# Kernel optimization log

Hardware: AMD Instinct MI355X
Metric: run time of the kernel (lower is better)

The kernel has to match this reference:

```python
import math
import jax, jax.numpy as jnp
import numpy as np

D_MODEL = 1024
D_FF = 4096
NUM_EXPERTS = 8
TOP_K = 2
CAP_FACTOR = 1.0
AUX_COEF = 0.01
Z_COEF = 0.0


def setup_inputs() -> dict:
    key = jax.random.key(0)
    ks = jax.random.split(key, 6)
    x = jax.random.normal(ks[0], (4, 2048, D_MODEL), dtype=jnp.float32)
    router_w = jax.random.normal(ks[1], (D_MODEL, NUM_EXPERTS), dtype=jnp.float32) / math.sqrt(D_MODEL)
    router_b = jnp.zeros((NUM_EXPERTS,), dtype=jnp.float32)
    w1 = jax.random.normal(ks[2], (NUM_EXPERTS, D_MODEL, D_FF), dtype=jnp.float32) / math.sqrt(D_MODEL)
    w3 = jax.random.normal(ks[3], (NUM_EXPERTS, D_MODEL, D_FF), dtype=jnp.float32) / math.sqrt(D_MODEL)
    w2 = jax.random.normal(ks[4], (NUM_EXPERTS, D_FF, D_MODEL), dtype=jnp.float32) / math.sqrt(D_FF)
    return {"x": x, "router_w": router_w, "router_b": router_b, "w1": w1, "w3": w3, "w2": w2}


def reference(x, router_w, router_b, w1, w3, w2):
    b, s, d = x.shape
    E, k = NUM_EXPERTS, TOP_K
    T = b * s
    x_flat = x.reshape(T, d)

    # ---- router ----
    logits = x_flat @ router_w + router_b                      # [T, E]
    logits_f32 = logits.astype(jnp.float32)
    probs = jax.nn.softmax(logits_f32, axis=-1)                # [T, E]
    topk_p, topk_i = jax.lax.top_k(probs, k)                   # [T, k]
    topk_p = topk_p / jnp.clip(topk_p.sum(-1, keepdims=True), 1e-9)  # normalize_gates
    gate = topk_p.reshape(-1)                                  # [T*k]
    expert_idx = topk_i.reshape(-1)                            # [T*k]

    # ---- aux loss (load balance + z-loss) ----
    importance = probs.mean(axis=0)                            # [E]
    load = jnp.bincount(topk_i[:, 0], length=E).astype(jnp.float32) / T
    lb_loss = (importance * load).sum() * float(E)
    z_loss = jnp.mean(jnp.square(jax.nn.logsumexp(logits_f32, axis=-1)))
    aux_loss = (AUX_COEF * lb_loss + Z_COEF * z_loss).astype(x.dtype)

    # ---- capacity-based dispatch ----
    N = T * k
    cap = max(1, int(math.ceil(CAP_FACTOR * N / E)))
    x_rep = jnp.repeat(x_flat, k, axis=0)                      # [N, d]
    order = jnp.argsort(expert_idx)                            # stable sort by expert
    e_sorted = expert_idx[order]
    x_sorted = x_rep[order]
    g_sorted = gate[order].astype(x.dtype)
    counts = jnp.bincount(e_sorted, length=E)
    starts = jnp.concatenate([jnp.zeros((1,), counts.dtype), jnp.cumsum(counts)[:-1]])
    pos = jnp.arange(N, dtype=counts.dtype) - starts[e_sorted]   # rank within expert group
    keep = pos < cap
    slot = jnp.where(keep, e_sorted * cap + pos, E * cap)      # dropped tokens -> dump row

    buf = jnp.zeros((E * cap + 1, d), dtype=x.dtype).at[slot].set(x_sorted)
    buf = buf[: E * cap].reshape(E, cap, d)                    # [E, C, d]

    # ---- grouped SwiGLU experts ----
    h = jax.nn.silu(jnp.einsum('ecd,edf->ecf', buf, w1)) * jnp.einsum('ecd,edf->ecf', buf, w3)
    y = jnp.einsum('ecf,efd->ecd', h, w2).reshape(E * cap, d)

    # ---- combine ----
    gathered = y[jnp.minimum(slot, E * cap - 1)]
    out_sorted = jnp.where(keep[:, None], gathered, 0.0) * g_sorted[:, None]
    inv = jnp.argsort(order)
    out = out_sorted[inv].reshape(T, k, d).sum(axis=1)
    return out.reshape(b, s, d), aux_loss
```

## Files before the change

### kernel.cpp

```cpp
#include <hip/hip_runtime.h>
#include <hip/hip_bf16.h>
#include <math.h>

constexpr int kT    = 8192;
constexpr int kD    = 1024;
constexpr int kF    = 4096;
constexpr int kE    = 8;
constexpr int kN    = kT * 2;
constexpr int kCap  = 2048;
constexpr int kECap = kE * kCap;

constexpr int kRouterBlocks = kT / 4;
constexpr int kT13Blocks    = (kF / 64) * (kD / 64) * 16;
constexpr int kT2Blocks     = (kD / 64) * (kF / 64) * 8;

typedef __attribute__((ext_vector_type(8))) short bf16x8;
typedef __attribute__((ext_vector_type(4))) float f32x4;

__device__ __forceinline__ void gload16(const __hip_bfloat16* g, __hip_bfloat16* l) {
  auto gp = (const __attribute__((address_space(1))) __hip_bfloat16*)g;
  auto lp = (__attribute__((address_space(3))) __hip_bfloat16*)l;
  __builtin_amdgcn_global_load_lds((const __attribute__((address_space(1))) void*)gp,
                                   (__attribute__((address_space(3))) void*)lp,
                                   16, 0, 0);
}

#define SYNC_VM(N) do { __builtin_amdgcn_sched_barrier(0); \
  asm volatile("s_waitcnt vmcnt(" #N ")" ::: "memory"); \
  __builtin_amdgcn_s_barrier(); \
  asm volatile("" ::: "memory"); } while (0)

__device__ __forceinline__ void transpose_body(const float* __restrict__ s,
                                               __hip_bfloat16* __restrict__ d,
                                               int R, int C, int bx, int by) {
  __shared__ float tile[64][65];
  const int c0 = bx * 64, r0 = by * 64;
  const int tid = threadIdx.x;
  const int lr = tid >> 4, lc4 = (tid & 15) * 4;
#pragma unroll
  for (int p = 0; p < 4; ++p) {
    int r = p * 16 + lr;
    float4 v = *(const float4*)(s + (size_t)(r0 + r) * C + c0 + lc4);
    tile[r][lc4] = v.x; tile[r][lc4 + 1] = v.y; tile[r][lc4 + 2] = v.z; tile[r][lc4 + 3] = v.w;
  }
  __syncthreads();
  const int c = tid >> 2, rc = (tid & 3) * 16;
  union { __hip_bfloat16 h[16]; bf16x8 v[2]; } o;
#pragma unroll
  for (int i = 0; i < 16; ++i) o.h[i] = __float2bfloat16(tile[rc + i][c]);
  __hip_bfloat16* drow = d + (size_t)(c0 + c) * R + r0 + rc;
  *(bf16x8*)drow = o.v[0];
  *(bf16x8*)(drow + 8) = o.v[1];
}

__global__ __launch_bounds__(256)
void prep_kernel(const float* __restrict__ x, const float* __restrict__ rw,
                 const float* __restrict__ rb, int* __restrict__ e_idx,
                 float* __restrict__ gates, float* __restrict__ probs_out,
                 const float* __restrict__ w1, const float* __restrict__ w3,
                 const float* __restrict__ w2, __hip_bfloat16* __restrict__ w1t,
                 __hip_bfloat16* __restrict__ w3t, __hip_bfloat16* __restrict__ w2t) {
  int bid = blockIdx.x;
  if (bid < kRouterBlocks) {
    int t = bid * 4 + (threadIdx.x >> 6);
    int lane = threadIdx.x & 63;
    const float* xr = x + (size_t)t * kD;
    float acc[8];
#pragma unroll
    for (int e = 0; e < 8; ++e) acc[e] = 0.f;
    for (int i = 0; i < kD / 256; ++i) {
      int d = i * 256 + lane * 4;
      float4 xv = *(const float4*)(xr + d);
#pragma unroll
      for (int j = 0; j < 4; ++j) {
        float xs = (j == 0) ? xv.x : (j == 1) ? xv.y : (j == 2) ? xv.z : xv.w;
        const float4* w4 = (const float4*)(rw + (size_t)(d + j) * 8);
        float4 wa = w4[0], wb = w4[1];
        acc[0] += xs * wa.x; acc[1] += xs * wa.y; acc[2] += xs * wa.z; acc[3] += xs * wa.w;
        acc[4] += xs * wb.x; acc[5] += xs * wb.y; acc[6] += xs * wb.z; acc[7] += xs * wb.w;
      }
    }
#pragma unroll
    for (int off = 32; off >= 1; off >>= 1) {
#pragma unroll
      for (int e = 0; e < 8; ++e) acc[e] += __shfl_xor(acc[e], off);
    }
    if (lane == 0) {
      float l[8], m = -1e30f;
#pragma unroll
      for (int e = 0; e < 8; ++e) { l[e] = acc[e] + rb[e]; m = fmaxf(m, l[e]); }
      float p[8], s = 0.f;
#pragma unroll
      for (int e = 0; e < 8; ++e) { p[e] = __expf(l[e] - m); s += p[e]; }
      float inv = 1.f / s;
#pragma unroll
      for (int e = 0; e < 8; ++e) p[e] *= inv;
      int i1 = 0;
#pragma unroll
      for (int e = 1; e < 8; ++e) if (p[e] > p[i1]) i1 = e;
      int i2 = (i1 == 0) ? 1 : 0;
#pragma unroll
      for (int e = 0; e < 8; ++e) if (e != i1 && e != i2 && p[e] > p[i2]) i2 = e;
      float den = fmaxf(p[i1] + p[i2], 1e-9f);
      e_idx[2 * t] = i1; e_idx[2 * t + 1] = i2;
      gates[2 * t] = p[i1] / den; gates[2 * t + 1] = p[i2] / den;
      float4* po = (float4*)(probs_out + (size_t)t * 8);
      po[0] = make_float4(p[0], p[1], p[2], p[3]);
      po[1] = make_float4(p[4], p[5], p[6], p[7]);
    }
    return;
  }
  const float* src; __hip_bfloat16* dst; int R, C, bx, by;
  bid -= kRouterBlocks;
  if (bid < kT13Blocks) {
    bx = bid & 63; by = (bid >> 6) & 15;
    int z = bid >> 10;
    R = kD; C = kF;
    size_t mat = (size_t)kD * kF;
    src = ((z < 8) ? w1 : w3) + (size_t)(z & 7) * mat;
    dst = ((z < 8) ? w1t : w3t) + (size_t)(z & 7) * mat;
  } else {
    bid -= kT13Blocks;
    bx = bid & 15; by = (bid >> 4) & 63;
    int e2 = bid >> 10;
    R = kF; C = kD;
    size_t mat = (size_t)kF * kD;
    src = w2 + (size_t)e2 * mat;
    dst = w2t + (size_t)e2 * mat;
  }
  transpose_body(src, dst, R, C, bx, by);
}

__global__ __launch_bounds__(1024)
void aux_kernel(const float* __restrict__ probs, const int* __restrict__ e_idx,
                float* __restrict__ aux_out) {
  int tid = threadIdx.x, lane = tid & 63, wave = tid >> 6;
  float imp[8];
  int cnt[8];
#pragma unroll
  for (int e = 0; e < 8; ++e) { imp[e] = 0.f; cnt[e] = 0; }
  for (int t = tid; t < kT; t += 1024) {
    const float4* p4 = (const float4*)(probs + (size_t)t * 8);
    float4 a = p4[0], b = p4[1];
    imp[0] += a.x; imp[1] += a.y; imp[2] += a.z; imp[3] += a.w;
    imp[4] += b.x; imp[5] += b.y; imp[6] += b.z; imp[7] += b.w;
    ++cnt[e_idx[2 * t] & 7];
  }
#pragma unroll
  for (int off = 32; off >= 1; off >>= 1) {
#pragma unroll
    for (int e = 0; e < 8; ++e) {
      imp[e] += __shfl_xor(imp[e], off);
      cnt[e] += __shfl_xor(cnt[e], off);
    }
  }
  __shared__ float simp[16][8];
  __shared__ int scnt[16][8];
  if (lane == 0) {
#pragma unroll
    for (int e = 0; e < 8; ++e) { simp[wave][e] = imp[e]; scnt[wave][e] = cnt[e]; }
  }
  __syncthreads();
  if (tid == 0) {
    float lb = 0.f;
    for (int e = 0; e < 8; ++e) {
      float I = 0.f; int C = 0;
      for (int w = 0; w < 16; ++w) { I += simp[w][e]; C += scnt[w][e]; }
      lb += (I / (float)kT) * ((float)C / (float)kT);
    }
    aux_out[0] = 0.01f * lb * (float)kE;
  }
}

__global__ __launch_bounds__(256)
void rank_kernel(const int* __restrict__ e_idx, int* __restrict__ slot_of,
                 int* __restrict__ token_of) {
  int e = blockIdx.x;
  __shared__ int wave_sum[4];
  __shared__ int running;
  int tid = threadIdx.x, lane = tid & 63, wave = tid >> 6;
  if (tid == 0) running = 0;
  __syncthreads();
  for (int base = 0; base < kN; base += 256) {
    int i = base + tid;
    bool f = (e_idx[i] == e);
    unsigned long long m = __ballot(f);
    int wpre = __popcll(m & ((1ull << lane) - 1ull));
    if (lane == 0) wave_sum[wave] = __popcll(m);
    __syncthreads();
    int woff = 0;
    for (int w = 0; w < wave; ++w) woff += wave_sum[w];
    int r = running;
    if (f) {
      int p = r + woff + wpre;
      if (p < kCap) {
        slot_of[i] = e * kCap + p;
        token_of[e * kCap + p] = i >> 1;
      } else {
        slot_of[i] = -1;
      }
    }
    __syncthreads();
    if (tid == 0) running = r + wave_sum[0] + wave_sum[1] + wave_sum[2] + wave_sum[3];
    __syncthreads();
  }
  for (int p = running + tid; p < kCap; p += 256)
    token_of[e * kCap + p] = -1;
}

struct __attribute__((aligned(8))) bf16x4s { __hip_bfloat16 v[4]; };

__global__ __launch_bounds__(64)
void gather_kernel(const float* __restrict__ x, const int* __restrict__ token_of,
                   __hip_bfloat16* __restrict__ buf) {
  int slot = blockIdx.x, lane = threadIdx.x;
  int t = token_of[slot];
  __hip_bfloat16* br = buf + (size_t)slot * kD;
  if (t >= 0) {
    const float* xr = x + (size_t)t * kD;
#pragma unroll
    for (int j = 0; j < 4; ++j) {
      int dd = (j * 64 + lane) * 4;
      float4 v = *(const float4*)(xr + dd);
      bf16x4s o;
      o.v[0] = __float2bfloat16(v.x); o.v[1] = __float2bfloat16(v.y);
      o.v[2] = __float2bfloat16(v.z); o.v[3] = __float2bfloat16(v.w);
      *(bf16x4s*)(br + dd) = o;
    }
  } else {
    bf16x4s z;
    z.v[0] = z.v[1] = z.v[2] = z.v[3] = __float2bfloat16(0.f);
#pragma unroll
    for (int j = 0; j < 4; ++j) *(bf16x4s*)(br + (j * 64 + lane) * 4) = z;
  }
}

__global__ __launch_bounds__(512, 2)
void gemm1_kernel(const __hip_bfloat16* __restrict__ Abase,
                  const __hip_bfloat16* __restrict__ W1t,
                  const __hip_bfloat16* __restrict__ W3t,
                  __hip_bfloat16* __restrict__ H) {
  constexpr int K = kD;
  constexpr int NT = K / 64;
  const int e = blockIdx.z, mt = blockIdx.y, ft = blockIdx.x;
  const int tid = threadIdx.x, lane = tid & 63, wave = tid >> 6;
  const int wr = wave >> 1, wc = wave & 1;
  const int frow = lane & 15, fk = lane >> 4;

  const __hip_bfloat16* A  = Abase + (size_t)(e * kCap + mt * 256) * K;
  const __hip_bfloat16* B1 = W1t + ((size_t)e * kF + ft * 128) * K;
  const __hip_bfloat16* B3 = W3t + ((size_t)e * kF + ft * 128) * K;

  extern __shared__ __hip_bfloat16 lds[];

  f32x4 accU[4][4], accV[4][4];
#pragma unroll
  for (int m = 0; m < 4; ++m)
#pragma unroll
    for (int n = 0; n < 4; ++n) {
      accU[m][n] = (f32x4){0.f, 0.f, 0.f, 0.f};
      accV[m][n] = (f32x4){0.f, 0.f, 0.f, 0.f};
    }

  auto stageA = [&](int t, int b) {
#pragma unroll
    for (int j = 0; j < 4; ++j) {
      int c = j * 128 + wc * 64 + lane;
      int rl = c >> 3, s = c & 7;
      const __hip_bfloat16* g = A + (size_t)(wr * 64 + rl) * K + t * 64 + (s ^ (rl & 7)) * 8;
      gload16(g, &lds[b * 32768 + wr * 4096 + (j * 128 + wc * 64) * 8]);
    }
  };
  auto stageB1 = [&](int t, int b) {
#pragma unroll
    for (int j = 0; j < 2; ++j) {
      int c = j * 256 + wr * 64 + lane;
      int rl = c >> 3, s = c & 7;
      const __hip_bfloat16* g = B1 + (size_t)(wc * 64 + rl) * K + t * 64 + (s ^ (rl & 7)) * 8;
      gload16(g, &lds[b * 32768 + 16384 + wc * 4096 + (j * 256 + wr * 64) * 8]);
    }
  };
  auto stageB3 = [&](int t, int b) {
#pragma unroll
    for (int j = 0; j < 2; ++j) {
      int c = j * 256 + wr * 64 + lane;
      int rl = c >> 3, s = c & 7;
      const __hip_bfloat16* g = B3 + (size_t)(wc * 64 + rl) * K + t * 64 + (s ^ (rl & 7)) * 8;
      gload16(g, &lds[b * 32768 + 16384 + 8192 + wc * 4096 + (j * 256 + wr * 64) * 8]);
    }
  };
  auto phase = [&](int b, f32x4 (&ac)[4][4], bf16x8 (&af)[4][2], int broff, bool loadA) {
    if (loadA) {
#pragma unroll
      for (int m = 0; m < 4; ++m)
#pragma unroll
        for (int h = 0; h < 2; ++h) {
          int row = wr * 64 + m * 16 + frow;
          af[m][h] = *(const bf16x8*)&lds[b * 32768 + row * 64 + ((h * 4 + fk) ^ (row & 7)) * 8];
        }
    }
    bf16x8 bf[4][2];
#pragma unroll
    for (int n = 0; n < 4; ++n)
#pragma unroll
      for (int h = 0; h < 2; ++h) {
        int row = broff + wc * 64 + n * 16 + frow;
        bf[n][h] = *(const bf16x8*)&lds[b * 32768 + 16384 + row * 64 + ((h * 4 + fk) ^ (row & 7)) * 8];
      }
    __builtin_amdgcn_s_setprio(1);
#pragma unroll
    for (int m = 0; m < 4; ++m)
#pragma unroll
      for (int n = 0; n < 4; ++n)
#pragma unroll
        for (int h = 0; h < 2; ++h)
          ac[m][n] = __builtin_amdgcn_mfma_f32_16x16x32_bf16(af[m][h], bf[n][h], ac[m][n], 0, 0, 0);
    __builtin_amdgcn_s_setprio(0);
    __builtin_amdgcn_sched_barrier(0);
  };

  stageA(0, 0); stageB1(0, 0); stageB3(0, 0);

  for (int t = 0; t < NT; ++t) {
    const int b = t & 1, nb = b ^ 1;
    const bool nx = (t + 1 < NT);
    SYNC_VM(2);
    if (nx) stageA(t + 1, nb);
    bf16x8 af[4][2];
    phase(b, accU, af, 0, true);
    if (nx) { SYNC_VM(4); } else { SYNC_VM(0); }
    if (nx) stageB1(t + 1, nb);
    phase(b, accV, af, 128, false);
    if (nx) stageB3(t + 1, nb);
  }

  __hip_bfloat16* Ht = H + (size_t)(e * kCap + mt * 256) * kF + ft * 128;
#pragma unroll
  for (int m = 0; m < 4; ++m)
#pragma unroll
    for (int n = 0; n < 4; ++n)
#pragma unroll
      for (int r = 0; r < 4; ++r) {
        int row = wr * 64 + m * 16 + fk * 4 + r;
        int col = wc * 64 + n * 16 + frow;
        float u = accU[m][n][r], v = accV[m][n][r];
        float hval = (u / (1.f + __expf(-u))) * v;
        Ht[(size_t)row * kF + col] = __float2bfloat16(hval);
      }
}

__global__ __launch_bounds__(512, 2)
void gemm2_kernel(const __hip_bfloat16* __restrict__ Hbase,
                  const __hip_bfloat16* __restrict__ W2t,
                  __hip_bfloat16* __restrict__ Y) {
  constexpr int K = kF;
  constexpr int NT = K / 64;
  const int e = blockIdx.z, mt = blockIdx.y, nt = blockIdx.x;
  const int tid = threadIdx.x, lane = tid & 63, wave = tid >> 6;
  const int wr = wave >> 2, wc = wave & 3;
  const int frow = lane & 15, fk = lane >> 4;

  const __hip_bfloat16* A = Hbase + (size_t)(e * kCap + mt * 256) * K;
  const __hip_bfloat16* B = W2t + ((size_t)e * kD + nt * 256) * K;

  extern __shared__ __hip_bfloat16 lds[];

  f32x4 acc[2][4][4];
#pragma unroll
  for (int p = 0; p < 2; ++p)
#pragma unroll
    for (int m = 0; m < 4; ++m)
#pragma unroll
      for (int n = 0; n < 4; ++n) acc[p][m][n] = (f32x4){0.f, 0.f, 0.f, 0.f};

  auto stageB = [&](int t, int b) {
#pragma unroll
    for (int j = 0; j < 4; ++j) {
      int c = j * 128 + wr * 64 + lane;
      int rl = c >> 3, s = c & 7;
      const __hip_bfloat16* g = B + (size_t)(wc * 64 + rl) * K + t * 64 + (s ^ (rl & 7)) * 8;
      gload16(g, &lds[b * 32768 + 16384 + wc * 4096 + (j * 128 + wr * 64) * 8]);
    }
  };
  auto stageA = [&](int t, int p, int b) {
    int q = 2 * wr + p;
#pragma unroll
    for (int j = 0; j < 2; ++j) {
      int c = j * 256 + wc * 64 + lane;
      int rl = c >> 3, s = c & 7;
      const __hip_bfloat16* g = A + (size_t)(q * 64 + rl) * K + t * 64 + (s ^ (rl & 7)) * 8;
      gload16(g, &lds[b * 32768 + q * 4096 + (j * 256 + wc * 64) * 8]);
    }
  };
  auto phase = [&](int b, int p, f32x4 (&ac)[4][4], bf16x8 (&bf)[4][2], bool loadB) {
    bf16x8 a[4][2];
#pragma unroll
    for (int m = 0; m < 4; ++m)
#pragma unroll
      for (int h = 0; h < 2; ++h) {
        int row = wr * 128 + p * 64 + m * 16 + frow;
        a[m][h] = *(const bf16x8*)&lds[b * 32768 + row * 64 + ((h * 4 + fk) ^ (row & 7)) * 8];
      }
    if (loadB) {
#pragma unroll
      for (int n = 0; n < 4; ++n)
#pragma unroll
        for (int h = 0; h < 2; ++h) {
          int row = wc * 64 + n * 16 + frow;
          bf[n][h] = *(const bf16x8*)&lds[b * 32768 + 16384 + row * 64 + ((h * 4 + fk) ^ (row & 7)) * 8];
        }
    }
    __builtin_amdgcn_s_setprio(1);
#pragma unroll
    for (int m = 0; m < 4; ++m)
#pragma unroll
      for (int n = 0; n < 4; ++n)
#pragma unroll
        for (int h = 0; h < 2; ++h)
          ac[m][n] = __builtin_amdgcn_mfma_f32_16x16x32_bf16(a[m][h], bf[n][h], ac[m][n], 0, 0, 0);
    __builtin_amdgcn_s_setprio(0);
    __builtin_amdgcn_sched_barrier(0);
  };

  stageB(0, 0); stageA(0, 0, 0); stageA(0, 1, 0);

  for (int t = 0; t < NT; ++t) {
    const int b = t & 1, nb = b ^ 1;
    const bool nx = (t + 1 < NT);
    SYNC_VM(2);
    if (nx) stageB(t + 1, nb);
    bf16x8 bf[4][2];
    phase(b, 0, acc[0], bf, true);
    if (nx) { SYNC_VM(4); } else { SYNC_VM(0); }
    if (nx) stageA(t + 1, 0, nb);
    phase(b, 1, acc[1], bf, false);
    if (nx) stageA(t + 1, 1, nb);
  }

  __hip_bfloat16* Yt = Y + (size_t)(e * kCap + mt * 256) * kD + nt * 256;
#pragma unroll
  for (int p = 0; p < 2; ++p)
#pragma unroll
    for (int m = 0; m < 4; ++m)
#pragma unroll
      for (int n = 0; n < 4; ++n)
#pragma unroll
        for (int r = 0; r < 4; ++r) {
          int row = wr * 128 + p * 64 + m * 16 + fk * 4 + r;
          int col = wc * 64 + n * 16 + frow;
          Yt[(size_t)row * kD + col] = __float2bfloat16(acc[p][m][n][r]);
        }
}

__global__ __launch_bounds__(256)
void combine_kernel(const __hip_bfloat16* __restrict__ Y, const int* __restrict__ slot_of,
                    const float* __restrict__ gates, float* __restrict__ out) {
  int t = blockIdx.x;
  int dd = threadIdx.x * 4;
  int s0 = slot_of[2 * t], s1 = slot_of[2 * t + 1];
  float g0 = gates[2 * t], g1 = gates[2 * t + 1];
  float4 r = {0.f, 0.f, 0.f, 0.f};
  if (s0 >= 0) {
    bf16x4s v = *(const bf16x4s*)(Y + (size_t)s0 * kD + dd);
    r.x += g0 * __bfloat162float(v.v[0]); r.y += g0 * __bfloat162float(v.v[1]);
    r.z += g0 * __bfloat162float(v.v[2]); r.w += g0 * __bfloat162float(v.v[3]);
  }
  if (s1 >= 0) {
    bf16x4s v = *(const bf16x4s*)(Y + (size_t)s1 * kD + dd);
    r.x += g1 * __bfloat162float(v.v[0]); r.y += g1 * __bfloat162float(v.v[1]);
    r.z += g1 * __bfloat162float(v.v[2]); r.w += g1 * __bfloat162float(v.v[3]);
  }
  *(float4*)(out + (size_t)t * kD + dd) = r;
}

extern "C" void kernel_launch(void* const* d_in, const int* in_sizes, int n_in,
                              void* d_out, int out_size, void* d_ws, size_t ws_size,
                              hipStream_t stream) {
  (void)in_sizes; (void)n_in; (void)out_size; (void)ws_size;
  const float* x  = (const float*)d_in[0];
  const float* rw = (const float*)d_in[1];
  const float* rb = (const float*)d_in[2];
  const float* w1 = (const float*)d_in[3];
  const float* w3 = (const float*)d_in[4];
  const float* w2 = (const float*)d_in[5];
  float* out = (float*)d_out;

  char* base = (char*)d_ws;
  size_t off = 0;
  auto alloc = [&](size_t bytes) -> char* {
    char* r = base + off;
    off += (bytes + 255) & ~(size_t)255;
    return r;
  };
  __hip_bfloat16* w1t = (__hip_bfloat16*)alloc((size_t)kE * kF * kD * 2);
  __hip_bfloat16* w3t = (__hip_bfloat16*)alloc((size_t)kE * kF * kD * 2);
  __hip_bfloat16* w2t = (__hip_bfloat16*)alloc((size_t)kE * kD * kF * 2);
  __hip_bfloat16* buf = (__hip_bfloat16*)alloc((size_t)kECap * kD * 2);
  __hip_bfloat16* h   = (__hip_bfloat16*)alloc((size_t)kECap * kF * 2);
  __hip_bfloat16* y   = (__hip_bfloat16*)alloc((size_t)kECap * kD * 2);
  int*   e_idx    = (int*)alloc((size_t)kN * 4);
  float* gates    = (float*)alloc((size_t)kN * 4);
  int*   slot_of  = (int*)alloc((size_t)kN * 4);
  int*   token_of = (int*)alloc((size_t)kECap * 4);
  float* probs    = (float*)alloc((size_t)kT * 8 * 4);

  prep_kernel<<<kRouterBlocks + kT13Blocks + kT2Blocks, 256, 0, stream>>>(
      x, rw, rb, e_idx, gates, probs, w1, w3, w2, w1t, w3t, w2t);
  aux_kernel<<<1, 1024, 0, stream>>>(probs, e_idx, out + (size_t)kT * kD);
  rank_kernel<<<kE, 256, 0, stream>>>(e_idx, slot_of, token_of);
  gather_kernel<<<kECap, 64, 0, stream>>>(x, token_of, buf);
  gemm1_kernel<<<dim3(kF / 128, kCap / 256, kE), 512, 131072, stream>>>(buf, w1t, w3t, h);
  gemm2_kernel<<<dim3(kD / 256, kCap / 256, kE), 512, 131072, stream>>>(h, w2t, y);
  combine_kernel<<<kT, 256, 0, stream>>>(y, slot_of, gates, out);
}
```

Before: 602.1 us.

## Switch expert GEMMs to single LDS buffer with register-staged prefetch

Both expert GEMM kernels drop double-buffered LDS in favour of a single buffer. Each k-step reads all A/B fragments into registers, barriers on LDS reads, then issues the global->LDS loads for the next tile and overlaps them with the MFMA block. Dynamic LDS per block is halved, which could raise occupancy. The cost is more fragment registers held at once and a full vmcnt(0) wait each iteration.

```diff
diff --git a/kernel.cpp b/kernel.cpp
--- a/kernel.cpp
+++ b/kernel.cpp
@@ -25,10 +25,14 @@
                                    16, 0, 0);
 }
 
-#define SYNC_VM(N) do { __builtin_amdgcn_sched_barrier(0); \
-  asm volatile("s_waitcnt vmcnt(" #N ")" ::: "memory"); \
+#define SYNC_VM0() do { __builtin_amdgcn_sched_barrier(0); \
+  asm volatile("s_waitcnt vmcnt(0)" ::: "memory"); \
   __builtin_amdgcn_s_barrier(); \
   asm volatile("" ::: "memory"); } while (0)
+#define READ_BARRIER() do { __builtin_amdgcn_sched_barrier(0); \
+  asm volatile("s_waitcnt lgkmcnt(0)" ::: "memory"); \
+  __builtin_amdgcn_s_barrier(); \
+  __builtin_amdgcn_sched_barrier(0); } while (0)
 
 __device__ __forceinline__ void transpose_body(const float* __restrict__ s,
                                                __hip_bfloat16* __restrict__ d,
@@ -262,51 +266,66 @@
       accV[m][n] = (f32x4){0.f, 0.f, 0.f, 0.f};
     }
 
-  auto stageA = [&](int t, int b) {
+  auto stageA = [&](int t) {
 #pragma unroll
     for (int j = 0; j < 4; ++j) {
       int c = j * 128 + wc * 64 + lane;
       int rl = c >> 3, s = c & 7;
       const __hip_bfloat16* g = A + (size_t)(wr * 64 + rl) * K + t * 64 + (s ^ (rl & 7)) * 8;
-      gload16(g, &lds[b * 32768 + wr * 4096 + (j * 128 + wc * 64) * 8]);
+      gload16(g, &lds[wr * 4096 + (j * 128 + wc * 64) * 8]);
     }
   };
-  auto stageB1 = [&](int t, int b) {
+  auto stageB1 = [&](int t) {
 #pragma unroll
     for (int j = 0; j < 2; ++j) {
       int c = j * 256 + wr * 64 + lane;
       int rl = c >> 3, s = c & 7;
       const __hip_bfloat16* g = B1 + (size_t)(wc * 64 + rl) * K + t * 64 + (s ^ (rl & 7)) * 8;
-      gload16(g, &lds[b * 32768 + 16384 + wc * 4096 + (j * 256 + wr * 64) * 8]);
+      gload16(g, &lds[16384 + wc * 4096 + (j * 256 + wr * 64) * 8]);
     }
   };
-  auto stageB3 = [&](int t, int b) {
+  auto stageB3 = [&](int t) {
 #pragma unroll
     for (int j = 0; j < 2; ++j) {
       int c = j * 256 + wr * 64 + lane;
       int rl = c >> 3, s = c & 7;
       const __hip_bfloat16* g = B3 + (size_t)(wc * 64 + rl) * K + t * 64 + (s ^ (rl & 7)) * 8;
-      gload16(g, &lds[b * 32768 + 16384 + 8192 + wc * 4096 + (j * 256 + wr * 64) * 8]);
+      gload16(g, &lds[16384 + 8192 + wc * 4096 + (j * 256 + wr * 64) * 8]);
     }
   };
-  auto phase = [&](int b, f32x4 (&ac)[4][4], bf16x8 (&af)[4][2], int broff, bool loadA) {
-    if (loadA) {
-#pragma unroll
-      for (int m = 0; m < 4; ++m)
-#pragma unroll
-        for (int h = 0; h < 2; ++h) {
-          int row = wr * 64 + m * 16 + frow;
-          af[m][h] = *(const bf16x8*)&lds[b * 32768 + row * 64 + ((h * 4 + fk) ^ (row & 7)) * 8];
-        }
-    }
-    bf16x8 bf[4][2];
+
+  stageA(0); stageB1(0); stageB3(0);
+
+  for (int t = 0; t < NT; ++t) {
+    const bool nx = (t + 1 < NT);
+    SYNC_VM0();
+
+    bf16x8 af[4][2], bu[4][2], bv[4][2];
+#pragma unroll
+    for (int m = 0; m < 4; ++m)
+#pragma unroll
+      for (int h = 0; h < 2; ++h) {
+        int row = wr * 64 + m * 16 + frow;
+        af[m][h] = *(const bf16x8*)&lds[row * 64 + ((h * 4 + fk) ^ (row & 7)) * 8];
+      }
 #pragma unroll
     for (int n = 0; n < 4; ++n)
 #pragma unroll
       for (int h = 0; h < 2; ++h) {
-        int row = broff + wc * 64 + n * 16 + frow;
-        bf[n][h] = *(const bf16x8*)&lds[b * 32768 + 16384 + row * 64 + ((h * 4 + fk) ^ (row & 7)) * 8];
-      }
+        int row = wc * 64 + n * 16 + frow;
+        bu[n][h] = *(const bf16x8*)&lds[16384 + row * 64 + ((h * 4 + fk) ^ (row & 7)) * 8];
+      }
+#pragma unroll
+    for (int n = 0; n < 4; ++n)
+#pragma unroll
+      for (int h = 0; h < 2; ++h) {
+        int row = 128 + wc * 64 + n * 16 + frow;
+        bv[n][h] = *(const bf16x8*)&lds[16384 + row * 64 + ((h * 4 + fk) ^ (row & 7)) * 8];
+      }
+    READ_BARRIER();
+
+    if (nx) { stageA(t + 1); stageB1(t + 1); stageB3(t + 1); }
+
     __builtin_amdgcn_s_setprio(1);
 #pragma unroll
     for (int m = 0; m < 4; ++m)
@@ -314,24 +333,16 @@
       for (int n = 0; n < 4; ++n)
 #pragma unroll
         for (int h = 0; h < 2; ++h)
-          ac[m][n] = __builtin_amdgcn_mfma_f32_16x16x32_bf16(af[m][h], bf[n][h], ac[m][n], 0, 0, 0);
+          accU[m][n] = __builtin_amdgcn_mfma_f32_16x16x32_bf16(af[m][h], bu[n][h], accU[m][n], 0, 0, 0);
+#pragma unroll
+    for (int m = 0; m < 4; ++m)
+#pragma unroll
+      for (int n = 0; n < 4; ++n)
+#pragma unroll
+        for (int h = 0; h < 2; ++h)
+          accV[m][n] = __builtin_amdgcn_mfma_f32_16x16x32_bf16(af[m][h], bv[n][h], accV[m][n], 0, 0, 0);
     __builtin_amdgcn_s_setprio(0);
     __builtin_amdgcn_sched_barrier(0);
-  };
-
-  stageA(0, 0); stageB1(0, 0); stageB3(0, 0);
-
-  for (int t = 0; t < NT; ++t) {
-    const int b = t & 1, nb = b ^ 1;
-    const bool nx = (t + 1 < NT);
-    SYNC_VM(2);
-    if (nx) stageA(t + 1, nb);
-    bf16x8 af[4][2];
-    phase(b, accU, af, 0, true);
-    if (nx) { SYNC_VM(4); } else { SYNC_VM(0); }
-    if (nx) stageB1(t + 1, nb);
-    phase(b, accV, af, 128, false);
-    if (nx) stageB3(t + 1, nb);
   }
 
   __hip_bfloat16* Ht = H + (size_t)(e * kCap + mt * 256) * kF + ft * 128;
@@ -373,68 +384,75 @@
 #pragma unroll
       for (int n = 0; n < 4; ++n) acc[p][m][n] = (f32x4){0.f, 0.f, 0.f, 0.f};
 
-  auto stageB = [&](int t, int b) {
+  auto stageB = [&](int t) {
 #pragma unroll
     for (int j = 0; j < 4; ++j) {
       int c = j * 128 + wr * 64 + lane;
       int rl = c >> 3, s = c & 7;
       const __hip_bfloat16* g = B + (size_t)(wc * 64 + rl) * K + t * 64 + (s ^ (rl & 7)) * 8;
-      gload16(g, &lds[b * 32768 + 16384 + wc * 4096 + (j * 128 + wr * 64) * 8]);
+      gload16(g, &lds[16384 + wc * 4096 + (j * 128 + wr * 64) * 8]);
     }
   };
-  auto stageA = [&](int t, int p, int b) {
+  auto stageA = [&](int t, int p) {
     int q = 2 * wr + p;
 #pragma unroll
     for (int j = 0; j < 2; ++j) {
       int c = j * 256 + wc * 64 + lane;
       int rl = c >> 3, s = c & 7;
       const __hip_bfloat16* g = A + (size_t)(q * 64 + rl) * K + t * 64 + (s ^ (rl & 7)) * 8;
-      gload16(g, &lds[b * 32768 + q * 4096 + (j * 256 + wc * 64) * 8]);
+      gload16(g, &lds[q * 4096 + (j * 256 + wc * 64) * 8]);
     }
   };
-  auto phase = [&](int b, int p, f32x4 (&ac)[4][4], bf16x8 (&bf)[4][2], bool loadB) {
-    bf16x8 a[4][2];
-#pragma unroll
-    for (int m = 0; m < 4; ++m)
+
+  stageB(0); stageA(0, 0); stageA(0, 1);
+
+  for (int t = 0; t < NT; ++t) {
+    const bool nx = (t + 1 < NT);
+    SYNC_VM0();
+
+    bf16x8 bf[4][2], a0[4][2], a1[4][2];
+#pragma unroll
+    for (int n = 0; n < 4; ++n)
 #pragma unroll
       for (int h = 0; h < 2; ++h) {
-        int row = wr * 128 + p * 64 + m * 16 + frow;
-        a[m][h] = *(const bf16x8*)&lds[b * 32768 + row * 64 + ((h * 4 + fk) ^ (row & 7)) * 8];
-      }
-    if (loadB) {
+        int row = wc * 64 + n * 16 + frow;
+        bf[n][h] = *(const bf16x8*)&lds[16384 + row * 64 + ((h * 4 + fk) ^ (row & 7)) * 8];
+      }
+#pragma unroll
+    for (int m = 0; m < 4; ++m)
+#pragma unroll
+      for (int h = 0; h < 2; ++h) {
+        int row = wr * 128 + m * 16 + frow;
+        a0[m][h] = *(const bf16x8*)&lds[row * 64 + ((h * 4 + fk) ^ (row & 7)) * 8];
+      }
+#pragma unroll
+    for (int m = 0; m < 4; ++m)
+#pragma unroll
+      for (int h = 0; h < 2; ++h) {
+        int row = wr * 128 + 64 + m * 16 + frow;
+        a1[m][h] = *(const bf16x8*)&lds[row * 64 + ((h * 4 + fk) ^ (row & 7)) * 8];
+      }
+    READ_BARRIER();
+
+    if (nx) { stageB(t + 1); stageA(t + 1, 0); stageA(t + 1, 1); }
+
+    __builtin_amdgcn_s_setprio(1);
+#pragma unroll
+    for (int m = 0; m < 4; ++m)
 #pragma unroll
       for (int n = 0; n < 4; ++n)
 #pragma unroll
-        for (int h = 0; h < 2; ++h) {
-          int row = wc * 64 + n * 16 + frow;
-          bf[n][h] = *(const bf16x8*)&lds[b * 32768 + 16384 + row * 64 + ((h * 4 + fk) ^ (row & 7)) * 8];
-        }
-    }
-    __builtin_amdgcn_s_setprio(1);
+        for (int h = 0; h < 2; ++h)
+          acc[0][m][n] = __builtin_amdgcn_mfma_f32_16x16x32_bf16(a0[m][h], bf[n][h], acc[0][m][n], 0, 0, 0);
 #pragma unroll
     for (int m = 0; m < 4; ++m)
 #pragma unroll
       for (int n = 0; n < 4; ++n)
 #pragma unroll
         for (int h = 0; h < 2; ++h)
-          ac[m][n] = __builtin_amdgcn_mfma_f32_16x16x32_bf16(a[m][h], bf[n][h], ac[m][n], 0, 0, 0);
+          acc[1][m][n] = __builtin_amdgcn_mfma_f32_16x16x32_bf16(a1[m][h], bf[n][h], acc[1][m][n], 0, 0, 0);
     __builtin_amdgcn_s_setprio(0);
     __builtin_amdgcn_sched_barrier(0);
-  };
-
-  stageB(0, 0); stageA(0, 0, 0); stageA(0, 1, 0);
-
-  for (int t = 0; t < NT; ++t) {
-    const int b = t & 1, nb = b ^ 1;
-    const bool nx = (t + 1 < NT);
-    SYNC_VM(2);
-    if (nx) stageB(t + 1, nb);
-    bf16x8 bf[4][2];
-    phase(b, 0, acc[0], bf, true);
-    if (nx) { SYNC_VM(4); } else { SYNC_VM(0); }
-    if (nx) stageA(t + 1, 0, nb);
-    phase(b, 1, acc[1], bf, false);
-    if (nx) stageA(t + 1, 1, nb);
   }
 
   __hip_bfloat16* Yt = Y + (size_t)(e * kCap + mt * 256) * kD + nt * 256;
@@ -509,7 +527,7 @@
   aux_kernel<<<1, 1024, 0, stream>>>(probs, e_idx, out + (size_t)kT * kD);
   rank_kernel<<<kE, 256, 0, stream>>>(e_idx, slot_of, token_of);
   gather_kernel<<<kECap, 64, 0, stream>>>(x, token_of, buf);
-  gemm1_kernel<<<dim3(kF / 128, kCap / 256, kE), 512, 131072, stream>>>(buf, w1t, w3t, h);
-  gemm2_kernel<<<dim3(kD / 256, kCap / 256, kE), 512, 131072, stream>>>(h, w2t, y);
+  gemm1_kernel<<<dim3(kF / 128, kCap / 256, kE), 512, 65536, stream>>>(buf, w1t, w3t, h);
+  gemm2_kernel<<<dim3(kD / 256, kCap / 256, kE), 512, 65536, stream>>>(h, w2t, y);
   combine_kernel<<<kT, 256, 0, stream>>>(y, slot_of, gates, out);
 }
```

New measurement: 752.6 us. +25.0%, slower.
